# Optimization experiments

Measured on AMD Instinct MI355X. Metric: run time of the kernel, lower is better.

## Reference

```python
import jax, jax.numpy as jnp
import numpy as np

SIG_LEVEL = 2
N_UNITS = 1024
INPUT_SIZE = 512
SIGSIZE = sum(2 ** k for k in range(1, SIG_LEVEL + 1))  # siglength(2, L) = 2^(L+1)-2 = 6
SAVED_LEN = N_UNITS * (1 + SIGSIZE)  # 7168
BATCH = 4096


def sigjoin(prev_sigs, disp, time_lapse, level):
    """Chen's identity: new_sig = prev_sig (tensor-mult) exp(v), truncated at `level`.

    prev_sigs: [N, SIGSIZE] flat signature levels (level k occupies 2^k entries),
    disp: [N, 1] displacement in dim 0; dim 1 displacement fixed to time_lapse.
    """
    N = prev_sigs.shape[0]
    v = jnp.concatenate([disp, jnp.full_like(disp, 1.0) * time_lapse], axis=1)  # [N, 2]
    # signature of the straight segment: seg_k = v^{(x)k} / k!
    seg = [v]
    for k in range(2, level + 1):
        seg.append((seg[-1][:, :, None] * v[:, None, :]).reshape(N, -1) / k)
    # split prev signature into levels
    S, off = [], 0
    for k in range(1, level + 1):
        sz = 2 ** k
        S.append(prev_sigs[:, off:off + sz])
        off += sz
    # result_k = S_k + seg_k + sum_{i=1}^{k-1} S_i (x) seg_{k-i}
    out = []
    for k in range(1, level + 1):
        r = S[k - 1] + seg[k - 1]
        for i in range(1, k):
            r = r + (S[i - 1][:, :, None] * seg[k - i - 1][:, None, :]).reshape(N, 2 ** k)
        out.append(r)
    return jnp.concatenate(out, axis=1)


def setup_inputs() -> dict:
    key = jax.random.key(0)
    ks = jax.random.split(key, 8)
    x = jax.random.normal(ks[0], (BATCH, INPUT_SIZE), dtype=jnp.float32)
    prev_sigs = jax.random.normal(ks[1], (BATCH, N_UNITS * SIGSIZE), dtype=jnp.float32) * 0.1
    prev_states = jax.random.normal(ks[2], (BATCH, N_UNITS), dtype=jnp.float32)
    W_w = jax.random.normal(ks[3], (N_UNITS, INPUT_SIZE), dtype=jnp.float32) / np.sqrt(INPUT_SIZE)
    W_b = jax.random.normal(ks[4], (N_UNITS,), dtype=jnp.float32) * 0.01
    U_w = jax.random.normal(ks[5], (N_UNITS, SAVED_LEN), dtype=jnp.float32) / np.sqrt(SAVED_LEN)
    U_b = jax.random.normal(ks[6], (N_UNITS,), dtype=jnp.float32) * 0.01
    log_timelapse = jnp.array([np.log(0.1)], dtype=jnp.float32)
    return {"x": x, "prev_sigs": prev_sigs, "prev_states": prev_states,
            "W_w": W_w, "W_b": W_b, "U_w": U_w, "U_b": U_b,
            "log_timelapse": log_timelapse}


def reference(x, prev_sigs, prev_states, W_w, W_b, U_w, U_b, log_timelapse):
    h = x @ W_w.T + W_b                                  # [B, n_units]
    mem = jnp.concatenate([prev_sigs, prev_states], 1)   # [B, saved_len]
    raw = h + mem @ U_w.T + U_b                          # [B, n_units]
    disp = (raw - prev_states).reshape(-1, 1)            # [B*n_units, 1]
    tl = jnp.exp(log_timelapse)[0]
    sigs = sigjoin(prev_sigs.reshape(-1, SIGSIZE), disp, tl, SIG_LEVEL)
    sigs = sigs.reshape(-1, N_UNITS * SIGSIZE)
    # output_signatures=True: output = [sigs, raw_output]
    return jnp.concatenate([sigs, raw], axis=1)          # [B, n_units*(sigsize+1)]
```

## Files before the change

### kernel.cpp

```cpp
#include <hip/hip_runtime.h>
#include <hip/hip_bf16.h>
#include <cmath>

#define BATCH   4096
#define NUNITS  1024
#define INSIZE  512
#define SIGSZ   6
#define KSIG    (NUNITS * SIGSZ)
#define SAVED   (KSIG + NUNITS)
#define KTOT    (INSIZE + KSIG + NUNITS)
#define OUTW    (NUNITS * (SIGSZ + 1))
#define NKT     (KTOT / 128)

#define WS_AX 0LL
#define WS_AS 2097152LL
#define WS_AT 27262976LL
#define WS_BW 31457280LL
#define WS_BU 31981568LL
#define WS_ELEMS 39321600LL
#define WS_BYTES (WS_ELEMS * 2)

typedef __attribute__((ext_vector_type(8)))  short bf16x8;
typedef __attribute__((ext_vector_type(8)))  unsigned short u16x8;
typedef __attribute__((ext_vector_type(4)))  float f32x4;
typedef __attribute__((ext_vector_type(16))) float f32x16;

__device__ __forceinline__ unsigned short f2bf(float f) {
    union { float f; unsigned int u; } c; c.f = f;
    unsigned int u = c.u;
    return (unsigned short)((u + 0x7FFFu + ((u >> 16) & 1u)) >> 16);
}
__device__ __forceinline__ float bf2f(unsigned short h) {
    union { unsigned int u; float f; } c; c.u = ((unsigned int)h) << 16;
    return c.f;
}

__global__ __launch_bounds__(256)
void prepack(const float* __restrict__ x, const float* __restrict__ sigs,
             const float* __restrict__ states, const float* __restrict__ Ww,
             const float* __restrict__ Uw, unsigned short* __restrict__ ws)
{
    const long long stride = (long long)gridDim.x * blockDim.x;
    for (long long p = (long long)blockIdx.x * blockDim.x + threadIdx.x;
         p < 4915200LL; p += stride) {
        const float* src; unsigned short* dst; long long o;
        if (p < 262144LL)       { src = x;      dst = ws + WS_AX; o = p; }
        else if (p < 3407872LL) { src = sigs;   dst = ws + WS_AS; o = p - 262144LL; }
        else if (p < 3932160LL) { src = states; dst = ws + WS_AT; o = p - 3407872LL; }
        else if (p < 3997696LL) { src = Ww;     dst = ws + WS_BW; o = p - 3932160LL; }
        else                    { src = Uw;     dst = ws + WS_BU; o = p - 3997696LL; }
        const f32x4 v0 = __builtin_nontemporal_load((const f32x4*)(src + o * 8));
        const f32x4 v1 = __builtin_nontemporal_load((const f32x4*)(src + o * 8) + 1);
        u16x8 h;
        h[0] = f2bf(v0[0]); h[1] = f2bf(v0[1]); h[2] = f2bf(v0[2]); h[3] = f2bf(v0[3]);
        h[4] = f2bf(v1[0]); h[5] = f2bf(v1[1]); h[6] = f2bf(v1[2]); h[7] = f2bf(v1[3]);
        *(u16x8*)(dst + o * 8) = h;
    }
}

#define GLD_LDS(G, L) __builtin_amdgcn_global_load_lds(                        \
        (const __attribute__((address_space(1))) unsigned int*)(G),           \
        (__attribute__((address_space(3))) unsigned int*)(L), 16, 0, 0)

__global__ __launch_bounds__(1024, 1)
void rsig_gemm(const unsigned short* __restrict__ ws,
               const float* __restrict__ states,
               const float* __restrict__ Wb,
               const float* __restrict__ Ub,
               const float* __restrict__ lt,
               float* __restrict__ out)
{
    __shared__ unsigned short lds[2 * 32768];

    const int t  = threadIdx.x;
    const int bn = blockIdx.x & 7;
    const int bm = blockIdx.x >> 3;

    const int lane = t & 63;
    const int w    = t >> 6;
    const int wm   = w >> 3;
    const int wn   = (w >> 2) & 1;
    const int wk   = w & 3;
    const int lrow = lane & 31;
    const int lhk  = lane >> 5;

    const unsigned short* wsAx = ws + WS_AX;
    const unsigned short* wsAs = ws + WS_AS;
    const unsigned short* wsAt = ws + WS_AT;
    const unsigned short* wsBw = ws + WS_BW;
    const unsigned short* wsBu = ws + WS_BU;

    const int sR4 = lane >> 4;
    const int sS  = lane & 15;

    f32x16 acc[2][2];
#pragma unroll
    for (int m = 0; m < 2; ++m)
#pragma unroll
        for (int n = 0; n < 2; ++n)
            acc[m][n] = (f32x16)0.f;

#define STAGE(BUF, KT)                                                                   \
    {                                                                                    \
        const int kt_ = (KT);                                                            \
        const unsigned short* abase; int astr; long long koff;                           \
        if (kt_ < 4)       { abase = wsAx; astr = INSIZE; koff = (long long)kt_*128; }   \
        else if (kt_ < 52) { abase = wsAs; astr = KSIG;   koff = (long long)kt_*128-512; }\
        else               { abase = wsAt; astr = NUNITS; koff = (long long)kt_*128-6656;}\
        const unsigned short* bbase; int bstr; long long koffb;                          \
        if (kt_ < 4)       { bbase = wsBw; bstr = INSIZE; koffb = (long long)kt_*128; }  \
        else               { bbase = wsBu; bstr = SAVED;  koffb = (long long)kt_*128-512;}\
        unsigned short* base = &lds[(BUF) * 32768];                                      \
        _Pragma("unroll")                                                                \
        for (int j = 0; j < 2; ++j) {                                                    \
            const int g    = 2 * w + j;                                                  \
            const int rT   = g * 4 + sR4;                                                \
            const int cblk = sS ^ (((g & 3) << 2) | sR4);                                \
            const unsigned short* ga = abase + (size_t)(bm * 128 + rT) * astr + koff + cblk * 8; \
            GLD_LDS(ga, base + g * 512);                                                 \
            const unsigned short* gb = bbase + (size_t)(bn * 128 + rT) * bstr + koffb + cblk * 8; \
            GLD_LDS(gb, base + 16384 + g * 512);                                         \
        }                                                                                \
    }

    STAGE(0, 0);

    for (int kt = 0; kt < NKT; ++kt) {
        asm volatile("s_waitcnt vmcnt(0)" ::: "memory");
        __builtin_amdgcn_s_barrier();
        __builtin_amdgcn_sched_barrier(0);

        const int cur = kt & 1;
        if (kt + 1 < NKT) STAGE(cur ^ 1, kt + 1);

        const unsigned short* aT = &lds[cur * 32768];
        const unsigned short* bT = aT + 16384;

        bf16x8 af[2][2], bfr[2][2];
#pragma unroll
        for (int m = 0; m < 2; ++m) {
            const int row = wm * 64 + m * 32 + lrow;
#pragma unroll
            for (int kk = 0; kk < 2; ++kk) {
                const int sg = wk * 4 + kk * 2 + lhk;
                af[m][kk] = *(const bf16x8*)&aT[row * 128 + ((sg ^ (row & 15)) << 3)];
            }
        }
#pragma unroll
        for (int n = 0; n < 2; ++n) {
            const int row = wn * 64 + n * 32 + lrow;
#pragma unroll
            for (int kk = 0; kk < 2; ++kk) {
                const int sg = wk * 4 + kk * 2 + lhk;
                bfr[n][kk] = *(const bf16x8*)&bT[row * 128 + ((sg ^ (row & 15)) << 3)];
            }
        }

#pragma unroll
        for (int kk = 0; kk < 2; ++kk)
#pragma unroll
            for (int m = 0; m < 2; ++m)
#pragma unroll
                for (int n = 0; n < 2; ++n)
                    acc[m][n] = __builtin_amdgcn_mfma_f32_32x32x16_bf16(
                        af[m][kk], bfr[n][kk], acc[m][n], 0, 0, 0);
    }

    __syncthreads();

    float* rawt = (float*)lds;
    const int ccol   = lane & 31;
    const int rowoff = 4 * lhk;
    if (wk == 0) {
#pragma unroll
        for (int m = 0; m < 2; ++m)
#pragma unroll
            for (int n = 0; n < 2; ++n) {
                const int cc = wn * 64 + n * 32 + ccol;
                const int rr = wm * 64 + m * 32 + rowoff;
                const float bias = Wb[bn * 128 + cc] + Ub[bn * 128 + cc];
#pragma unroll
                for (int reg = 0; reg < 16; ++reg) {
                    const int r = rr + (reg & 3) + 8 * (reg >> 2);
                    rawt[r * 132 + cc] = acc[m][n][reg] + bias;
                }
            }
    }
    __syncthreads();
#pragma unroll
    for (int slot = 1; slot < 4; ++slot) {
        if (wk == slot) {
#pragma unroll
            for (int m = 0; m < 2; ++m)
#pragma unroll
                for (int n = 0; n < 2; ++n) {
                    const int cc = wn * 64 + n * 32 + ccol;
                    const int rr = wm * 64 + m * 32 + rowoff;
#pragma unroll
                    for (int reg = 0; reg < 16; ++reg) {
                        const int r = rr + (reg & 3) + 8 * (reg >> 2);
                        rawt[r * 132 + cc] += acc[m][n][reg];
                    }
                }
        }
        __syncthreads();
    }

    const float tl = expf(lt[0]);
    const int r0 = t >> 8;
    const int c  = t & 255;

    for (int pass = 0; pass < 32; ++pass) {
        const int r = pass * 4 + r0;
        const long long b = (long long)bm * 128 + r;
        if (c < 192) {
            const int u  = (2 * c) / 3;
            const int cs = c % 3;
            const unsigned short* srow = wsAs + b * KSIG + bn * 768;
            const float* strow = states + b * NUNITS + bn * 128;
            const ushort4 sin = *(const ushort4*)(srow + c * 4);
            const float e0 = bf2f(sin.x), e1 = bf2f(sin.y);
            const float e2 = bf2f(sin.z), e3 = bf2f(sin.w);
            float4 o;
            if (cs == 0) {
                const float d = rawt[r * 132 + u] - strow[u];
                o.x = e0 + d;
                o.y = e1 + tl;
                o.z = e2 + d  * (0.5f * d  + e0);
                o.w = e3 + tl * (0.5f * d  + e0);
            } else if (cs == 1) {
                const float d  = rawt[r * 132 + u]     - strow[u];
                const float dn = rawt[r * 132 + u + 1] - strow[u + 1];
                const float s1 = bf2f(srow[u * 6 + 1]);
                o.x = e0 + d  * (0.5f * tl + s1);
                o.y = e1 + tl * (0.5f * tl + s1);
                o.z = e2 + dn;
                o.w = e3 + tl;
            } else {
                const float d = rawt[r * 132 + u] - strow[u];
                const unsigned int sv = *(const unsigned int*)(srow + u * 6);
                const float s0 = bf2f((unsigned short)(sv & 0xffffu));
                const float s1 = bf2f((unsigned short)(sv >> 16));
                o.x = e0 + d  * (0.5f * d  + s0);
                o.y = e1 + tl * (0.5f * d  + s0);
                o.z = e2 + d  * (0.5f * tl + s1);
                o.w = e3 + tl * (0.5f * tl + s1);
            }
            *(float4*)(out + b * OUTW + bn * 768 + c * 4) = o;
        } else if (c < 224) {
            const int cc = (c - 192) * 4;
            const float4 rv = *(const float4*)&rawt[r * 132 + cc];
            *(float4*)(out + b * OUTW + KSIG + bn * 128 + cc) = rv;
        }
    }
#undef STAGE
}

extern "C" void kernel_launch(void* const* d_in, const int* in_sizes, int n_in,
                              void* d_out, int out_size, void* d_ws, size_t ws_size,
                              hipStream_t stream) {
    const float* x      = (const float*)d_in[0];
    const float* sigs   = (const float*)d_in[1];
    const float* states = (const float*)d_in[2];
    const float* Ww     = (const float*)d_in[3];
    const float* Wb     = (const float*)d_in[4];
    const float* Uw     = (const float*)d_in[5];
    const float* Ub     = (const float*)d_in[6];
    const float* lt     = (const float*)d_in[7];
    float* out = (float*)d_out;

    unsigned short* ws = (unsigned short*)d_ws;
    hipLaunchKernelGGL(prepack, dim3(2048), dim3(256), 0, stream,
                       x, sigs, states, Ww, Uw, ws);
    hipLaunchKernelGGL(rsig_gemm, dim3(256), dim3(1024), 0, stream,
                       ws, states, Wb, Ub, lt, out);
}
```

Before: 179.0 us.

## Switch GEMM main loop to triple-buffered K=64 tiles with prefetch depth two

The K tile is halved from 128 to 64, and LDS goes from two buffers to three, so loads for tile kt+2 are issued while tile kt is computed. The wait becomes vmcnt(2) instead of vmcnt(0), which keeps one stage's global loads in flight across the barrier. The LDS layout and XOR swizzle are redone for 64-wide rows packed two per 128-element line. The cost is twice as many loop iterations and barriers, each doing half the MFMA work.

```diff
diff --git a/kernel.cpp b/kernel.cpp
--- a/kernel.cpp
+++ b/kernel.cpp
@@ -10,7 +10,7 @@
 #define SAVED   (KSIG + NUNITS)
 #define KTOT    (INSIZE + KSIG + NUNITS)
 #define OUTW    (NUNITS * (SIGSZ + 1))
-#define NKT     (KTOT / 128)
+#define NKT     (KTOT / 64)
 
 #define WS_AX 0LL
 #define WS_AS 2097152LL
@@ -70,7 +70,7 @@
                const float* __restrict__ lt,
                float* __restrict__ out)
 {
-    __shared__ unsigned short lds[2 * 32768];
+    __shared__ unsigned short lds[3 * 16384];
 
     const int t  = threadIdx.x;
     const int bn = blockIdx.x & 7;
@@ -82,7 +82,8 @@
     const int wn   = (w >> 2) & 1;
     const int wk   = w & 3;
     const int lrow = lane & 31;
-    const int lhk  = lane >> 5;
+    const int lkh  = lane >> 5;
+    const int kbw  = wk * 2 + lkh;
 
     const unsigned short* wsAx = ws + WS_AX;
     const unsigned short* wsAs = ws + WS_AS;
@@ -90,8 +91,10 @@
     const unsigned short* wsBw = ws + WS_BW;
     const unsigned short* wsBu = ws + WS_BU;
 
-    const int sR4 = lane >> 4;
-    const int sS  = lane & 15;
+    const int sD   = w * 4 + (lane >> 4);
+    const int sKey = (lane & 15) ^ (sD & 15);
+    const int sR   = sD * 2 + (sKey & 1);
+    const int sKb  = sKey >> 1;
 
     f32x16 acc[2][2];
 #pragma unroll
@@ -104,73 +107,66 @@
     {                                                                                    \
         const int kt_ = (KT);                                                            \
         const unsigned short* abase; int astr; long long koff;                           \
-        if (kt_ < 4)       { abase = wsAx; astr = INSIZE; koff = (long long)kt_*128; }   \
-        else if (kt_ < 52) { abase = wsAs; astr = KSIG;   koff = (long long)kt_*128-512; }\
-        else               { abase = wsAt; astr = NUNITS; koff = (long long)kt_*128-6656;}\
+        if (kt_ < 8)        { abase = wsAx; astr = INSIZE; koff = kt_ * 64LL; }          \
+        else if (kt_ < 104) { abase = wsAs; astr = KSIG;   koff = kt_ * 64LL - 512; }    \
+        else                { abase = wsAt; astr = NUNITS; koff = kt_ * 64LL - 6656; }   \
         const unsigned short* bbase; int bstr; long long koffb;                          \
-        if (kt_ < 4)       { bbase = wsBw; bstr = INSIZE; koffb = (long long)kt_*128; }  \
-        else               { bbase = wsBu; bstr = SAVED;  koffb = (long long)kt_*128-512;}\
-        unsigned short* base = &lds[(BUF) * 32768];                                      \
-        _Pragma("unroll")                                                                \
-        for (int j = 0; j < 2; ++j) {                                                    \
-            const int g    = 2 * w + j;                                                  \
-            const int rT   = g * 4 + sR4;                                                \
-            const int cblk = sS ^ (((g & 3) << 2) | sR4);                                \
-            const unsigned short* ga = abase + (size_t)(bm * 128 + rT) * astr + koff + cblk * 8; \
-            GLD_LDS(ga, base + g * 512);                                                 \
-            const unsigned short* gb = bbase + (size_t)(bn * 128 + rT) * bstr + koffb + cblk * 8; \
-            GLD_LDS(gb, base + 16384 + g * 512);                                         \
-        }                                                                                \
+        if (kt_ < 8)        { bbase = wsBw; bstr = INSIZE; koffb = kt_ * 64LL; }         \
+        else                { bbase = wsBu; bstr = SAVED;  koffb = kt_ * 64LL - 512; }   \
+        unsigned short* base = &lds[(BUF) * 16384];                                      \
+        GLD_LDS(abase + (size_t)(bm * 128 + sR) * astr + koff  + sKb * 8, base + w * 512);        \
+        GLD_LDS(bbase + (size_t)(bn * 128 + sR) * bstr + koffb + sKb * 8, base + 8192 + w * 512); \
     }
 
     STAGE(0, 0);
-
+    STAGE(1, 1);
+
+    int cur = 0;
     for (int kt = 0; kt < NKT; ++kt) {
-        asm volatile("s_waitcnt vmcnt(0)" ::: "memory");
+        if (kt < NKT - 1) { asm volatile("s_waitcnt vmcnt(2)" ::: "memory"); }
+        else              { asm volatile("s_waitcnt vmcnt(0)" ::: "memory"); }
         __builtin_amdgcn_s_barrier();
         __builtin_amdgcn_sched_barrier(0);
 
-        const int cur = kt & 1;
-        if (kt + 1 < NKT) STAGE(cur ^ 1, kt + 1);
-
-        const unsigned short* aT = &lds[cur * 32768];
-        const unsigned short* bT = aT + 16384;
-
-        bf16x8 af[2][2], bfr[2][2];
-#pragma unroll
-        for (int m = 0; m < 2; ++m) {
-            const int row = wm * 64 + m * 32 + lrow;
-#pragma unroll
-            for (int kk = 0; kk < 2; ++kk) {
-                const int sg = wk * 4 + kk * 2 + lhk;
-                af[m][kk] = *(const bf16x8*)&aT[row * 128 + ((sg ^ (row & 15)) << 3)];
-            }
-        }
-#pragma unroll
-        for (int n = 0; n < 2; ++n) {
-            const int row = wn * 64 + n * 32 + lrow;
-#pragma unroll
-            for (int kk = 0; kk < 2; ++kk) {
-                const int sg = wk * 4 + kk * 2 + lhk;
-                bfr[n][kk] = *(const bf16x8*)&bT[row * 128 + ((sg ^ (row & 15)) << 3)];
-            }
-        }
-
-#pragma unroll
-        for (int kk = 0; kk < 2; ++kk)
+        if (kt + 2 < NKT) {
+            int nb = cur + 2; if (nb >= 3) nb -= 3;
+            STAGE(nb, kt + 2);
+        }
+
+        {
+            const unsigned short* aT = &lds[cur * 16384];
+            const unsigned short* bT = aT + 8192;
+            bf16x8 af[2], bfr[2];
+#pragma unroll
+            for (int m = 0; m < 2; ++m) {
+                const int R = wm * 64 + m * 32 + lrow;
+                const int D = R >> 1;
+                const int s = ((kbw << 1) | (R & 1)) ^ (D & 15);
+                af[m] = *(const bf16x8*)&aT[D * 128 + s * 8];
+            }
+#pragma unroll
+            for (int n = 0; n < 2; ++n) {
+                const int R = wn * 64 + n * 32 + lrow;
+                const int D = R >> 1;
+                const int s = ((kbw << 1) | (R & 1)) ^ (D & 15);
+                bfr[n] = *(const bf16x8*)&bT[D * 128 + s * 8];
+            }
 #pragma unroll
             for (int m = 0; m < 2; ++m)
 #pragma unroll
                 for (int n = 0; n < 2; ++n)
                     acc[m][n] = __builtin_amdgcn_mfma_f32_32x32x16_bf16(
-                        af[m][kk], bfr[n][kk], acc[m][n], 0, 0, 0);
+                        af[m], bfr[n], acc[m][n], 0, 0, 0);
+        }
+
+        cur = (cur == 2) ? 0 : cur + 1;
     }
 
     __syncthreads();
 
     float* rawt = (float*)lds;
     const int ccol   = lane & 31;
-    const int rowoff = 4 * lhk;
+    const int rowoff = 4 * lkh;
     if (wk == 0) {
 #pragma unroll
         for (int m = 0; m < 2; ++m)
```

After: 172.6 us. 3.6% less time.
